# Kernel tuning notes

Hardware: AMD Instinct MI355X
Metric: run time of the kernel (lower is better)

## Reference

```python
import jax, jax.numpy as jnp
import numpy as np

E = 512
H = 8
DH = E // H
LN_EPS = 1e-5


def setup_inputs() -> dict:
    key = jax.random.key(0)
    ks = jax.random.split(key, 8)
    s = 1.0 / np.sqrt(E)
    return {
        "query": jax.random.normal(ks[0], (2, 2048, E), jnp.float32),
        "key_value": jax.random.normal(ks[1], (2, 4096, E), jnp.float32),
        "Wq": jax.random.normal(ks[2], (E, E), jnp.float32) * s,
        "bq": jnp.zeros((E,), jnp.float32),
        "Wk": jax.random.normal(ks[3], (E, E), jnp.float32) * s,
        "bk": jnp.zeros((E,), jnp.float32),
        "Wv": jax.random.normal(ks[4], (E, E), jnp.float32) * s,
        "bv": jnp.zeros((E,), jnp.float32),
        "Wo": jax.random.normal(ks[5], (E, E), jnp.float32) * s,
        "bo": jnp.zeros((E,), jnp.float32),
        "ln_gamma": jnp.ones((E,), jnp.float32),
        "ln_beta": jnp.zeros((E,), jnp.float32),
    }


def reference(query, key_value, Wq, bq, Wk, bk, Wv, bv, Wo, bo, ln_gamma, ln_beta):
    B, Lq, _ = query.shape
    Lk = key_value.shape[1]
    # Projections (torch Linear: x @ W.T + b)
    q = (query @ Wq.T + bq).reshape(B, Lq, H, DH)
    k = (key_value @ Wk.T + bk).reshape(B, Lk, H, DH)
    v = (key_value @ Wv.T + bv).reshape(B, Lk, H, DH)
    scale = 1.0 / np.sqrt(DH).astype(np.float32)
    scores = jnp.einsum("bqhd,bkhd->bhqk", q, k) * scale  # [B,H,Lq,Lk]
    attn = jax.nn.softmax(scores, axis=-1)
    ctx = jnp.einsum("bhqk,bkhd->bqhd", attn, v).reshape(B, Lq, E)
    attn_out = ctx @ Wo.T + bo
    # residual + LayerNorm (dropout is identity in eval)
    x = query + attn_out
    mu = jnp.mean(x, axis=-1, keepdims=True)
    var = jnp.mean(jnp.square(x - mu), axis=-1, keepdims=True)
    return (x - mu) * jax.lax.rsqrt(var + LN_EPS) * ln_gamma + ln_beta
```

## Files before the change

### kernel.cpp

```cpp
#include <hip/hip_runtime.h>
#include <hip/hip_bf16.h>

typedef __bf16 bf16;
typedef __bf16 bf16x8 __attribute__((ext_vector_type(8)));
typedef __bf16 bf16x4 __attribute__((ext_vector_type(4)));
typedef float f32x4 __attribute__((ext_vector_type(4)));
typedef float f32x16 __attribute__((ext_vector_type(16)));
typedef unsigned int u32x4 __attribute__((ext_vector_type(4)));

#define MFMA16(a, b, c) __builtin_amdgcn_mfma_f32_16x16x32_bf16((a), (b), (c), 0, 0, 0)
#define MFMA32(a, b, c) __builtin_amdgcn_mfma_f32_32x32x16_bf16((a), (b), (c), 0, 0, 0)

constexpr int LQ = 2048, LK = 4096, E = 512, H = 8, DH = 64;
#define QSCALE 0.1803368801111137f

#if __has_builtin(__builtin_amdgcn_exp2f)
#define EXP2(x) __builtin_amdgcn_exp2f(x)
#else
#define EXP2(x) __expf(0.6931471805599453f * (x))
#endif

__device__ __forceinline__ bf16x8 ld8(const bf16* p) { return *(const bf16x8*)p; }

__global__ __launch_bounds__(256) void cvt4_kernel(
    const float* __restrict__ w0, const float* __restrict__ w1,
    const float* __restrict__ w2, const float* __restrict__ w3,
    bf16* __restrict__ dst) {
  const float* srcs[4] = {w0, w1, w2, w3};
  const float* src = srcs[blockIdx.y];
  bf16* d = dst + (size_t)blockIdx.y * 262144;
  int i = (blockIdx.x * 256 + threadIdx.x) * 4;
  f32x4 v = *(const f32x4*)(src + i);
  bf16x4 o;
  for (int j = 0; j < 4; ++j) o[j] = (bf16)v[j];
  *(bf16x4*)(d + i) = o;
}

__global__ __launch_bounds__(256) void proj_gemm_kernel(
    const float* __restrict__ query, const float* __restrict__ kv,
    const bf16* __restrict__ Wall,
    const float* __restrict__ bq, const float* __restrict__ bk,
    const float* __restrict__ bv,
    bf16* __restrict__ qproj, bf16* __restrict__ kproj, bf16* __restrict__ vt) {
  __shared__ bf16 smA[2][128][72];
  __shared__ bf16 smB[2][128][72];
  const int tid = threadIdx.x;
  const int lane = tid & 63, wave = tid >> 6;
  const int lrow = lane & 15, quad = lane >> 4;
  const int wm = wave & 1, wn = wave >> 1;

  int x = blockIdx.x, z, mt;
  if (x < 32) { z = 0; mt = x; }
  else if (x < 96) { z = 1; mt = x - 32; }
  else { z = 2; mt = x - 96; }
  const float* A = ((z == 0) ? query : kv) + (size_t)mt * 128 * E;
  const bf16* W = Wall + (size_t)z * 262144;
  const float* bias = (z == 0) ? bq : (z == 1) ? bk : bv;
  const int n0 = blockIdx.y * 128;

  const int arow = tid >> 4, acol = tid & 15;
  const int brow = tid >> 3, bcol = tid & 7;

  f32x4 pa[8];
  bf16x8 pb[4];
#define LOAD_T(t)                                                             \
  {                                                                           \
    for (int p = 0; p < 8; ++p)                                               \
      pa[p] = *(const f32x4*)(A + (size_t)(p * 16 + arow) * E + (t) * 64 +    \
                              acol * 4);                                      \
    for (int p = 0; p < 4; ++p)                                               \
      pb[p] = ld8(W + (size_t)(n0 + p * 32 + brow) * E + (t) * 64 + bcol * 8);\
  }
#define STORE_T(bs)                                                           \
  {                                                                           \
    for (int p = 0; p < 8; ++p) {                                             \
      bf16x4 av;                                                              \
      for (int e = 0; e < 4; ++e) av[e] = (bf16)pa[p][e];                     \
      *(bf16x4*)&smA[bs][p * 16 + arow][acol * 4] = av;                       \
    }                                                                         \
    for (int p = 0; p < 4; ++p)                                               \
      *(bf16x8*)&smB[bs][p * 32 + brow][bcol * 8] = pb[p];                    \
  }

  LOAD_T(0);
  STORE_T(0);
  LOAD_T(1);
  __syncthreads();

  f32x4 acc[4][4] = {};
  for (int t = 0; t < 8; ++t) {
    const int bs = t & 1;
    bf16x8 af[2][4], bfr[2][4];
    for (int ks = 0; ks < 2; ++ks)
      for (int i = 0; i < 4; ++i)
        af[ks][i] = ld8(&smA[bs][wm * 64 + 16 * i + lrow][ks * 32 + quad * 8]);
    for (int ks = 0; ks < 2; ++ks)
      for (int c = 0; c < 4; ++c)
        bfr[ks][c] = ld8(&smB[bs][wn * 64 + 16 * c + lrow][ks * 32 + quad * 8]);
    for (int ks = 0; ks < 2; ++ks)
      for (int i = 0; i < 4; ++i)
        for (int c = 0; c < 4; ++c)
          acc[i][c] = MFMA16(af[ks][i], bfr[ks][c], acc[i][c]);
    if (t < 7) {
      STORE_T(bs ^ 1);
      if (t < 6) LOAD_T(t + 2);
    }
    __syncthreads();
  }
#undef LOAD_T
#undef STORE_T

  const float qsc = (z == 0) ? QSCALE : 1.f;
  float bvl[4];
  for (int c = 0; c < 4; ++c) bvl[c] = bias[n0 + wn * 64 + 16 * c + lrow];
  bf16* Cs = &smA[0][0][0];
  for (int i = 0; i < 4; ++i)
    for (int c = 0; c < 4; ++c)
      for (int r = 0; r < 4; ++r) {
        int row = wm * 64 + 16 * i + 4 * quad + r;
        int col = wn * 64 + 16 * c + lrow;
        bf16 val = (bf16)((acc[i][c][r] + bvl[c]) * qsc);
        if (z < 2) Cs[row * 136 + col] = val;
        else       Cs[col * 136 + row] = val;
      }
  __syncthreads();
  const int rr = tid >> 1, hh = tid & 1;
  if (z < 2) {
    bf16* Y = (z == 0) ? qproj : kproj;
    bf16* dstp = Y + (size_t)(mt * 128 + rr) * E + n0 + hh * 64;
    for (int j = 0; j < 8; ++j)
      *(bf16x8*)(dstp + j * 8) = *(bf16x8*)&Cs[rr * 136 + hh * 64 + j * 8];
  } else {
    int m0g = mt * 128, b = m0g >> 12, kk0 = m0g & 4095;
    int ng = n0 + rr, hd = ng >> 6, d = ng & 63;
    bf16* dstp = vt + ((size_t)((b * 8 + hd) * 64 + d)) * LK + kk0 + hh * 64;
    for (int j = 0; j < 8; ++j)
      *(bf16x8*)(dstp + j * 8) = *(bf16x8*)&Cs[rr * 136 + hh * 64 + j * 8];
  }
}

__global__ __launch_bounds__(256, 2) void attn_kernel(
    const bf16* __restrict__ qp, const bf16* __restrict__ kp,
    const bf16* __restrict__ vtg, bf16* __restrict__ ctx) {
  const int tid = threadIdx.x;
  const int lane = tid & 63, wave = tid >> 6;
  const int l31 = lane & 31, hi = lane >> 5;
  const int hw = blockIdx.x;
  const int xcd = hw & 7, ii = hw >> 3;
  const int bh = xcd * 2 + (ii >> 5), qt = ii & 31;
  const int b = bh >> 3, h = bh & 7;
  const int q0 = qt * 64;

  __shared__ __align__(16) char smem[70656];
  bf16* Ks = (bf16*)(smem + wave * 8192);
  bf16* Vs = Ks + 2048;

  bf16x8 qf[2][4];
  for (int t = 0; t < 2; ++t)
    for (int st = 0; st < 4; ++st)
      qf[t][st] = ld8(qp + (size_t)(b * LQ + q0 + 32 * t + l31) * E + h * DH +
                      st * 16 + hi * 8);

  float lp[2] = {0.f, 0.f};
  f32x16 acc[2][2] = {};

  const int kkbase = wave * 1024;
  const int krow_ = lane >> 3, kg_ = lane & 7;
  const int vrow_ = lane >> 2, vg_ = lane & 3;
  const bf16* kgp =
      kp + ((size_t)b * LK + kkbase + krow_) * E + h * DH + kg_ * 8;
  const bf16* vgp = vtg + ((size_t)bh * DH + vrow_) * LK + kkbase + vg_ * 8;
  const int kws = (kg_ ^ krow_) * 8;
  const int vws = (vg_ ^ (vrow_ & 3)) * 8;

  bf16x8 pk[4], pv[4];
#define GLOAD(it)                                                   \
  for (int j = 0; j < 4; ++j) {                                     \
    pk[j] = ld8(kgp + ((size_t)(it)*32 + j * 8) * E);               \
    pv[j] = ld8(vgp + (size_t)j * 16 * LK + (it)*32);               \
  }
#define STAGE()                                                     \
  for (int j = 0; j < 4; ++j) {                                     \
    *(bf16x8*)&Ks[(j * 8 + krow_) * 64 + kws] = pk[j];              \
    *(bf16x8*)&Vs[(j * 16 + vrow_) * 32 + vws] = pv[j];             \
  }

  GLOAD(0);
  STAGE();
  for (int it = 0; it < 32; ++it) {
    if (it < 31) GLOAD(it + 1);

    bf16x8 kf[4], vf[2][2];
#pragma unroll
    for (int st = 0; st < 4; ++st)
      kf[st] = ld8(&Ks[l31 * 64 + ((st * 2 + hi) ^ (l31 & 7)) * 8]);
#pragma unroll
    for (int dt = 0; dt < 2; ++dt)
      for (int s = 0; s < 2; ++s)
        vf[dt][s] =
            ld8(&Vs[(dt * 32 + l31) * 32 + ((s * 2 + hi) ^ (l31 & 3)) * 8]);

#pragma unroll
    for (int t = 0; t < 2; ++t) {
      f32x16 s_ = {};
      __builtin_amdgcn_s_setprio(1);
      s_ = MFMA32(kf[0], qf[t][0], s_);
      s_ = MFMA32(kf[1], qf[t][1], s_);
      s_ = MFMA32(kf[2], qf[t][2], s_);
      s_ = MFMA32(kf[3], qf[t][3], s_);
      __builtin_amdgcn_s_setprio(0);
      unsigned w[4][2];
#pragma unroll
      for (int t4 = 0; t4 < 4; ++t4)
#pragma unroll
        for (int u = 0; u < 2; ++u) {
          float e0 = EXP2(s_[4 * t4 + 2 * u]);
          float e1 = EXP2(s_[4 * t4 + 2 * u + 1]);
          lp[t] += e0;
          lp[t] += e1;
          asm("v_cvt_pk_bf16_f32 %0, %1, %2"
              : "=v"(w[t4][u])
              : "v"(e0), "v"(e1));
        }
      bf16x8 paf[2];
#pragma unroll
      for (int s = 0; s < 2; ++s) {
        unsigned a0 = w[2 * s][0], b0 = w[2 * s + 1][0];
        unsigned a1 = w[2 * s][1], b1 = w[2 * s + 1][1];
        asm("v_permlane32_swap_b32 %0, %1" : "+v"(a0), "+v"(b0));
        asm("v_permlane32_swap_b32 %0, %1" : "+v"(a1), "+v"(b1));
        u32x4 pw_ = {a0, a1, b0, b1};
        paf[s] = *(bf16x8*)&pw_;
      }
      __builtin_amdgcn_s_setprio(1);
#pragma unroll
      for (int dt = 0; dt < 2; ++dt)
        for (int s = 0; s < 2; ++s)
          acc[t][dt] = MFMA32(paf[s], vf[dt][s], acc[t][dt]);
      __builtin_amdgcn_s_setprio(0);

      if (t == 0 && it < 31) STAGE();
    }
  }
#undef GLOAD
#undef STAGE

  for (int t = 0; t < 2; ++t) lp[t] += __shfl_xor(lp[t], 32);

  __syncthreads();
  float* F = (float*)smem;
  float* Lr = (float*)(smem + 69632);
#pragma unroll
  for (int t = 0; t < 2; ++t)
    for (int dt = 0; dt < 2; ++dt)
#pragma unroll
      for (int r = 0; r < 16; ++r) {
        int q = 32 * t + (r & 3) + 8 * (r >> 2) + 4 * hi;
        F[(wave * 64 + q) * 68 + dt * 32 + l31] = acc[t][dt][r];
      }
  if (hi == 0) {
    Lr[wave * 64 + l31] = lp[0];
    Lr[wave * 64 + 32 + l31] = lp[1];
  }
  __syncthreads();
  {
    const int q = tid >> 2, d0 = (tid & 3) * 16;
    float ls = Lr[q] + Lr[64 + q] + Lr[128 + q] + Lr[192 + q];
    float inv = 1.f / ls;
    float o[16] = {};
    for (int w2 = 0; w2 < 4; ++w2) {
      const float* Fr = &F[(w2 * 64 + q) * 68 + d0];
      for (int j = 0; j < 16; j += 4) {
        f32x4 x = *(const f32x4*)(Fr + j);
        o[j] += x[0];
        o[j + 1] += x[1];
        o[j + 2] += x[2];
        o[j + 3] += x[3];
      }
    }
    bf16* dst = ctx + (size_t)(b * LQ + q0 + q) * E + h * DH + d0;
    bf16x8 ov0, ov1;
    for (int j = 0; j < 8; ++j) {
      ov0[j] = (bf16)(o[j] * inv);
      ov1[j] = (bf16)(o[8 + j] * inv);
    }
    *(bf16x8*)dst = ov0;
    *(bf16x8*)(dst + 8) = ov1;
  }
}

__global__ __launch_bounds__(512) void outln_kernel(
    const bf16* __restrict__ Cx, const bf16* __restrict__ Wo,
    const float* __restrict__ bo, const float* __restrict__ resid,
    const float* __restrict__ gamma, const float* __restrict__ beta,
    float* __restrict__ out) {
  const int tid = threadIdx.x;
  const int lane = tid & 63, wave = tid >> 6;
  const int lrow = lane & 15, quad = lane >> 4;
  const int m0 = blockIdx.x * 16;
  const int n0 = wave * 64;

  __shared__ bf16 As[16][520];
  __shared__ bf16 Wos[512][72];
  __shared__ float red1[16][8], red2[16][8];
  {
    int r = tid >> 5, ch = tid & 31;
    const bf16* src = Cx + (size_t)(m0 + r) * E + ch * 16;
    *(bf16x8*)&As[r][ch * 16] = ld8(src);
    *(bf16x8*)&As[r][ch * 16 + 8] = ld8(src + 8);
  }
  const int wr = tid >> 3, wc = tid & 7;
  bf16x8 pw[8];
  for (int p = 0; p < 8; ++p)
    pw[p] = ld8(Wo + (size_t)(p * 64 + wr) * E + wc * 8);
  __syncthreads();

  f32x4 acc[4] = {};
  for (int t = 0; t < 8; ++t) {
    for (int p = 0; p < 8; ++p)
      *(bf16x8*)&Wos[p * 64 + wr][wc * 8] = pw[p];
    __syncthreads();
    if (t < 7)
      for (int p = 0; p < 8; ++p)
        pw[p] = ld8(Wo + (size_t)(p * 64 + wr) * E + (t + 1) * 64 + wc * 8);
    for (int ks = 0; ks < 2; ++ks) {
      bf16x8 a = *(const bf16x8*)&As[lrow][t * 64 + ks * 32 + quad * 8];
      for (int c = 0; c < 4; ++c) {
        bf16x8 w = *(const bf16x8*)&Wos[n0 + 16 * c + lrow][ks * 32 + quad * 8];
        acc[c] = MFMA16(a, w, acc[c]);
      }
    }
    __syncthreads();
  }

  float s1[4] = {}, s2[4] = {};
  for (int c = 0; c < 4; ++c) {
    int n = n0 + 16 * c + lrow;
    float bb = bo[n];
    for (int r = 0; r < 4; ++r) {
      int m = 4 * quad + r;
      float xv = acc[c][r] + bb + resid[(size_t)(m0 + m) * E + n];
      acc[c][r] = xv;
      s1[r] += xv;
      s2[r] += xv * xv;
    }
  }
  for (int off = 1; off < 16; off <<= 1)
    for (int r = 0; r < 4; ++r) {
      s1[r] += __shfl_xor(s1[r], off);
      s2[r] += __shfl_xor(s2[r], off);
    }
  if (lrow == 0)
    for (int r = 0; r < 4; ++r) {
      red1[4 * quad + r][wave] = s1[r];
      red2[4 * quad + r][wave] = s2[r];
    }
  __syncthreads();
  float mu[4], rstd[4];
  for (int r = 0; r < 4; ++r) {
    int m = 4 * quad + r;
    float t1 = 0.f, t2 = 0.f;
    for (int w = 0; w < 8; ++w) { t1 += red1[m][w]; t2 += red2[m][w]; }
    float mean = t1 * (1.f / 512.f);
    float var = t2 * (1.f / 512.f) - mean * mean;
    mu[r] = mean;
    rstd[r] = rsqrtf(var + 1e-5f);
  }
  for (int c = 0; c < 4; ++c) {
    int n = n0 + 16 * c + lrow;
    float gm = gamma[n], bt = beta[n];
    for (int r = 0; r < 4; ++r) {
      int m = m0 + 4 * quad + r;
      out[(size_t)m * E + n] = (acc[c][r] - mu[r]) * rstd[r] * gm + bt;
    }
  }
}

extern "C" void kernel_launch(void* const* d_in, const int* in_sizes, int n_in,
                              void* d_out, int out_size, void* d_ws, size_t ws_size,
                              hipStream_t stream) {
  const float* query     = (const float*)d_in[0];
  const float* key_value = (const float*)d_in[1];
  const float* Wq = (const float*)d_in[2];
  const float* bq = (const float*)d_in[3];
  const float* Wk = (const float*)d_in[4];
  const float* bk = (const float*)d_in[5];
  const float* Wv = (const float*)d_in[6];
  const float* bv = (const float*)d_in[7];
  const float* Wo = (const float*)d_in[8];
  const float* bo = (const float*)d_in[9];
  const float* gamma = (const float*)d_in[10];
  const float* beta  = (const float*)d_in[11];
  float* out = (float*)d_out;

  bf16* Wb    = (bf16*)d_ws;
  bf16* Wob   = Wb + (size_t)3 * 262144;
  bf16* qproj = Wb + (size_t)4 * 262144;
  bf16* kproj = qproj + (size_t)4096 * 512;
  bf16* vt    = kproj + (size_t)8192 * 512;

  cvt4_kernel<<<dim3(256, 4), 256, 0, stream>>>(Wq, Wk, Wv, Wo, Wb);
  proj_gemm_kernel<<<dim3(160, 4), 256, 0, stream>>>(
      query, key_value, Wb, bq, bk, bv, qproj, kproj, vt);
  attn_kernel<<<512, 256, 0, stream>>>(qproj, kproj, vt, qproj );
  outln_kernel<<<256, 512, 0, stream>>>(qproj, Wob, bo, query, gamma, beta, out);
}
```

Measured before the change: 176.2 us.

## Load K/V MFMA fragments directly from global memory with register double-buffering

The attention inner loop no longer stages K and V tiles through per-wave shared memory. Each lane now loads its MFMA operand fragments straight from global memory into two register sets that alternate across iterations. This removes the LDS write/read traffic and swizzle address math, but the global loads are less coalesced, since each lane reads 16-byte pieces from separate rows. It also raises register pressure, which could affect occupancy under the 2-wave-per-SIMD launch bound.

Result: slower. 193.4 us (+9.7%).

```diff
diff --git a/kernel.cpp b/kernel.cpp
--- a/kernel.cpp
+++ b/kernel.cpp
@@ -152,8 +152,6 @@
   const int q0 = qt * 64;
 
   __shared__ __align__(16) char smem[70656];
-  bf16* Ks = (bf16*)(smem + wave * 8192);
-  bf16* Vs = Ks + 2048;
 
   bf16x8 qf[2][4];
   for (int t = 0; t < 2; ++t)
@@ -165,85 +163,75 @@
   f32x16 acc[2][2] = {};
 
   const int kkbase = wave * 1024;
-  const int krow_ = lane >> 3, kg_ = lane & 7;
-  const int vrow_ = lane >> 2, vg_ = lane & 3;
-  const bf16* kgp =
-      kp + ((size_t)b * LK + kkbase + krow_) * E + h * DH + kg_ * 8;
-  const bf16* vgp = vtg + ((size_t)bh * DH + vrow_) * LK + kkbase + vg_ * 8;
-  const int kws = (kg_ ^ krow_) * 8;
-  const int vws = (vg_ ^ (vrow_ & 3)) * 8;
-
-  bf16x8 pk[4], pv[4];
-#define GLOAD(it)                                                   \
-  for (int j = 0; j < 4; ++j) {                                     \
-    pk[j] = ld8(kgp + ((size_t)(it)*32 + j * 8) * E);               \
-    pv[j] = ld8(vgp + (size_t)j * 16 * LK + (it)*32);               \
-  }
-#define STAGE()                                                     \
-  for (int j = 0; j < 4; ++j) {                                     \
-    *(bf16x8*)&Ks[(j * 8 + krow_) * 64 + kws] = pk[j];              \
-    *(bf16x8*)&Vs[(j * 16 + vrow_) * 32 + vws] = pv[j];             \
-  }
-
-  GLOAD(0);
-  STAGE();
-  for (int it = 0; it < 32; ++it) {
-    if (it < 31) GLOAD(it + 1);
-
-    bf16x8 kf[4], vf[2][2];
-#pragma unroll
-    for (int st = 0; st < 4; ++st)
-      kf[st] = ld8(&Ks[l31 * 64 + ((st * 2 + hi) ^ (l31 & 7)) * 8]);
-#pragma unroll
-    for (int dt = 0; dt < 2; ++dt)
-      for (int s = 0; s < 2; ++s)
-        vf[dt][s] =
-            ld8(&Vs[(dt * 32 + l31) * 32 + ((s * 2 + hi) ^ (l31 & 3)) * 8]);
-
-#pragma unroll
-    for (int t = 0; t < 2; ++t) {
-      f32x16 s_ = {};
-      __builtin_amdgcn_s_setprio(1);
-      s_ = MFMA32(kf[0], qf[t][0], s_);
-      s_ = MFMA32(kf[1], qf[t][1], s_);
-      s_ = MFMA32(kf[2], qf[t][2], s_);
-      s_ = MFMA32(kf[3], qf[t][3], s_);
-      __builtin_amdgcn_s_setprio(0);
-      unsigned w[4][2];
-#pragma unroll
-      for (int t4 = 0; t4 < 4; ++t4)
-#pragma unroll
-        for (int u = 0; u < 2; ++u) {
-          float e0 = EXP2(s_[4 * t4 + 2 * u]);
-          float e1 = EXP2(s_[4 * t4 + 2 * u + 1]);
-          lp[t] += e0;
-          lp[t] += e1;
-          asm("v_cvt_pk_bf16_f32 %0, %1, %2"
-              : "=v"(w[t4][u])
-              : "v"(e0), "v"(e1));
-        }
-      bf16x8 paf[2];
-#pragma unroll
-      for (int s = 0; s < 2; ++s) {
-        unsigned a0 = w[2 * s][0], b0 = w[2 * s + 1][0];
-        unsigned a1 = w[2 * s][1], b1 = w[2 * s + 1][1];
-        asm("v_permlane32_swap_b32 %0, %1" : "+v"(a0), "+v"(b0));
-        asm("v_permlane32_swap_b32 %0, %1" : "+v"(a1), "+v"(b1));
-        u32x4 pw_ = {a0, a1, b0, b1};
-        paf[s] = *(bf16x8*)&pw_;
-      }
-      __builtin_amdgcn_s_setprio(1);
-#pragma unroll
-      for (int dt = 0; dt < 2; ++dt)
-        for (int s = 0; s < 2; ++s)
-          acc[t][dt] = MFMA32(paf[s], vf[dt][s], acc[t][dt]);
-      __builtin_amdgcn_s_setprio(0);
-
-      if (t == 0 && it < 31) STAGE();
-    }
-  }
-#undef GLOAD
-#undef STAGE
+  const bf16* kfb =
+      kp + ((size_t)b * LK + kkbase + l31) * E + h * DH + hi * 8;
+  const bf16* vfb = vtg + ((size_t)bh * DH + l31) * LK + kkbase + hi * 8;
+
+#define LOADT(kf_, vf_, it)                                          \
+  {                                                                  \
+    const bf16* kpp = kfb + (size_t)(it) * 32 * E;                   \
+    kf_[0] = ld8(kpp);                                               \
+    kf_[1] = ld8(kpp + 16);                                          \
+    kf_[2] = ld8(kpp + 32);                                          \
+    kf_[3] = ld8(kpp + 48);                                          \
+    const bf16* vpp = vfb + (it) * 32;                               \
+    vf_[0] = ld8(vpp);                                               \
+    vf_[1] = ld8(vpp + 16);                                          \
+    vf_[2] = ld8(vpp + (size_t)32 * LK);                             \
+    vf_[3] = ld8(vpp + (size_t)32 * LK + 16);                        \
+  }
+
+#define COMPUTE(kf_, vf_)                                            \
+  _Pragma("unroll")                                                  \
+  for (int t = 0; t < 2; ++t) {                                      \
+    f32x16 s_ = {};                                                  \
+    __builtin_amdgcn_s_setprio(1);                                   \
+    s_ = MFMA32(kf_[0], qf[t][0], s_);                               \
+    s_ = MFMA32(kf_[1], qf[t][1], s_);                               \
+    s_ = MFMA32(kf_[2], qf[t][2], s_);                               \
+    s_ = MFMA32(kf_[3], qf[t][3], s_);                               \
+    __builtin_amdgcn_s_setprio(0);                                   \
+    unsigned w_[4][2];                                               \
+    _Pragma("unroll")                                                \
+    for (int t4 = 0; t4 < 4; ++t4)                                   \
+      _Pragma("unroll")                                              \
+      for (int u = 0; u < 2; ++u) {                                  \
+        float e0 = EXP2(s_[4 * t4 + 2 * u]);                         \
+        float e1 = EXP2(s_[4 * t4 + 2 * u + 1]);                     \
+        lp[t] += e0;                                                 \
+        lp[t] += e1;                                                 \
+        asm("v_cvt_pk_bf16_f32 %0, %1, %2"                           \
+            : "=v"(w_[t4][u])                                        \
+            : "v"(e0), "v"(e1));                                     \
+      }                                                              \
+    bf16x8 paf[2];                                                   \
+    _Pragma("unroll")                                                \
+    for (int s = 0; s < 2; ++s) {                                    \
+      unsigned a0 = w_[2 * s][0], b0 = w_[2 * s + 1][0];             \
+      unsigned a1 = w_[2 * s][1], b1 = w_[2 * s + 1][1];             \
+      asm("v_permlane32_swap_b32 %0, %1" : "+v"(a0), "+v"(b0));      \
+      asm("v_permlane32_swap_b32 %0, %1" : "+v"(a1), "+v"(b1));      \
+      u32x4 pw_ = {a0, a1, b0, b1};                                  \
+      paf[s] = *(bf16x8*)&pw_;                                       \
+    }                                                                \
+    __builtin_amdgcn_s_setprio(1);                                   \
+    acc[t][0] = MFMA32(paf[0], vf_[0], acc[t][0]);                   \
+    acc[t][0] = MFMA32(paf[1], vf_[1], acc[t][0]);                   \
+    acc[t][1] = MFMA32(paf[0], vf_[2], acc[t][1]);                   \
+    acc[t][1] = MFMA32(paf[1], vf_[3], acc[t][1]);                   \
+    __builtin_amdgcn_s_setprio(0);                                   \
+  }
+
+  bf16x8 kfA[4], vfA[4], kfB[4], vfB[4];
+  LOADT(kfA, vfA, 0);
+  for (int it = 0; it < 32; it += 2) {
+    LOADT(kfB, vfB, it + 1);
+    COMPUTE(kfA, vfA);
+    if (it + 2 < 32) LOADT(kfA, vfA, it + 2);
+    COMPUTE(kfB, vfB);
+  }
+#undef LOADT
+#undef COMPUTE
 
   for (int t = 0; t < 2; ++t) lp[t] += __shfl_xor(lp[t], 32);
 
```

## Split attention key range across eight waves per block with two-pass reduction

Applied to the files above, without the earlier changes.

Each attention block now runs 512 threads (8 waves) instead of 256, and each wave covers 512 keys instead of 1024, halving the serial loop length per wave. The cross-wave reduction of partial outputs is done in two passes, one per 32-column half of the head dimension, using a narrower padded LDS buffer so shared memory does not grow. The aim is more in-flight waves per CU to hide load and MFMA latency. In exchange the kernel adds an extra reduction pass and barriers, and the tighter launch bound may force fewer registers per thread and cause spills.

New measurement: 512.4 us. +190.7%, slower.

```diff
diff --git a/kernel.cpp b/kernel.cpp
--- a/kernel.cpp
+++ b/kernel.cpp
@@ -139,7 +139,7 @@
   }
 }
 
-__global__ __launch_bounds__(256, 2) void attn_kernel(
+__global__ __launch_bounds__(512, 4) void attn_kernel(
     const bf16* __restrict__ qp, const bf16* __restrict__ kp,
     const bf16* __restrict__ vtg, bf16* __restrict__ ctx) {
   const int tid = threadIdx.x;
@@ -151,7 +151,7 @@
   const int b = bh >> 3, h = bh & 7;
   const int q0 = qt * 64;
 
-  __shared__ __align__(16) char smem[70656];
+  __shared__ __align__(16) char smem[69632];
   bf16* Ks = (bf16*)(smem + wave * 8192);
   bf16* Vs = Ks + 2048;
 
@@ -164,7 +164,7 @@
   float lp[2] = {0.f, 0.f};
   f32x16 acc[2][2] = {};
 
-  const int kkbase = wave * 1024;
+  const int kkbase = wave * 512;
   const int krow_ = lane >> 3, kg_ = lane & 7;
   const int vrow_ = lane >> 2, vg_ = lane & 3;
   const bf16* kgp =
@@ -187,8 +187,8 @@
 
   GLOAD(0);
   STAGE();
-  for (int it = 0; it < 32; ++it) {
-    if (it < 31) GLOAD(it + 1);
+  for (int it = 0; it < 16; ++it) {
+    if (it < 15) GLOAD(it + 1);
 
     bf16x8 kf[4], vf[2][2];
 #pragma unroll
@@ -239,7 +239,7 @@
           acc[t][dt] = MFMA32(paf[s], vf[dt][s], acc[t][dt]);
       __builtin_amdgcn_s_setprio(0);
 
-      if (t == 0 && it < 31) STAGE();
+      if (t == 0 && it < 15) STAGE();
     }
   }
 #undef GLOAD
@@ -249,43 +249,54 @@
 
   __syncthreads();
   float* F = (float*)smem;
-  float* Lr = (float*)(smem + 69632);
-#pragma unroll
-  for (int t = 0; t < 2; ++t)
-    for (int dt = 0; dt < 2; ++dt)
-#pragma unroll
-      for (int r = 0; r < 16; ++r) {
-        int q = 32 * t + (r & 3) + 8 * (r >> 2) + 4 * hi;
-        F[(wave * 64 + q) * 68 + dt * 32 + l31] = acc[t][dt][r];
-      }
+  float* Lr = (float*)(smem + 67584);
   if (hi == 0) {
     Lr[wave * 64 + l31] = lp[0];
     Lr[wave * 64 + 32 + l31] = lp[1];
   }
-  __syncthreads();
+#pragma unroll
+  for (int t = 0; t < 2; ++t)
+#pragma unroll
+    for (int r = 0; r < 16; ++r) {
+      int q = 32 * t + (r & 3) + 8 * (r >> 2) + 4 * hi;
+      F[(wave * 64 + q) * 33 + l31] = acc[t][0][r];
+    }
+  __syncthreads();
+  const int mq = tid >> 3, d0 = (tid & 7) * 4;
+  float ls = 0.f;
+#pragma unroll
+  for (int w2 = 0; w2 < 8; ++w2) ls += Lr[w2 * 64 + mq];
+  const float inv = 1.f / ls;
   {
-    const int q = tid >> 2, d0 = (tid & 3) * 16;
-    float ls = Lr[q] + Lr[64 + q] + Lr[128 + q] + Lr[192 + q];
-    float inv = 1.f / ls;
-    float o[16] = {};
-    for (int w2 = 0; w2 < 4; ++w2) {
-      const float* Fr = &F[(w2 * 64 + q) * 68 + d0];
-      for (int j = 0; j < 16; j += 4) {
-        f32x4 x = *(const f32x4*)(Fr + j);
-        o[j] += x[0];
-        o[j + 1] += x[1];
-        o[j + 2] += x[2];
-        o[j + 3] += x[3];
-      }
-    }
-    bf16* dst = ctx + (size_t)(b * LQ + q0 + q) * E + h * DH + d0;
-    bf16x8 ov0, ov1;
-    for (int j = 0; j < 8; ++j) {
-      ov0[j] = (bf16)(o[j] * inv);
-      ov1[j] = (bf16)(o[8 + j] * inv);
-    }
-    *(bf16x8*)dst = ov0;
-    *(bf16x8*)(dst + 8) = ov1;
+    float o[4] = {0.f, 0.f, 0.f, 0.f};
+#pragma unroll
+    for (int w2 = 0; w2 < 8; ++w2) {
+      const float* Fr = &F[(w2 * 64 + mq) * 33 + d0];
+      for (int j = 0; j < 4; ++j) o[j] += Fr[j];
+    }
+    bf16x4 ov;
+    for (int j = 0; j < 4; ++j) ov[j] = (bf16)(o[j] * inv);
+    *(bf16x4*)(ctx + (size_t)(b * LQ + q0 + mq) * E + h * DH + d0) = ov;
+  }
+  __syncthreads();
+#pragma unroll
+  for (int t = 0; t < 2; ++t)
+#pragma unroll
+    for (int r = 0; r < 16; ++r) {
+      int q = 32 * t + (r & 3) + 8 * (r >> 2) + 4 * hi;
+      F[(wave * 64 + q) * 33 + l31] = acc[t][1][r];
+    }
+  __syncthreads();
+  {
+    float o[4] = {0.f, 0.f, 0.f, 0.f};
+#pragma unroll
+    for (int w2 = 0; w2 < 8; ++w2) {
+      const float* Fr = &F[(w2 * 64 + mq) * 33 + d0];
+      for (int j = 0; j < 4; ++j) o[j] += Fr[j];
+    }
+    bf16x4 ov;
+    for (int j = 0; j < 4; ++j) ov[j] = (bf16)(o[j] * inv);
+    *(bf16x4*)(ctx + (size_t)(b * LQ + q0 + mq) * E + h * DH + 32 + d0) = ov;
   }
 }
 
@@ -402,6 +413,6 @@
   cvt4_kernel<<<dim3(256, 4), 256, 0, stream>>>(Wq, Wk, Wv, Wo, Wb);
   proj_gemm_kernel<<<dim3(160, 4), 256, 0, stream>>>(
       query, key_value, Wb, bq, bk, bv, qproj, kproj, vt);
-  attn_kernel<<<512, 256, 0, stream>>>(qproj, kproj, vt, qproj );
+  attn_kernel<<<512, 512, 0, stream>>>(qproj, kproj, vt, qproj );
   outln_kernel<<<256, 512, 0, stream>>>(qproj, Wob, bo, query, gamma, beta, out);
 }
```
